# Kernel optimization log

Hardware: AMD Instinct MI355X
Metric: run time of the kernel (lower is better)

## Reference

```python
import jax, jax.numpy as jnp
import numpy as np

SEQ_LEN = 1024
DIM = 384
QK_DIM = 64
BATCH = 16


def setup_inputs() -> dict:
    key = jax.random.key(0)
    k_x, k_qw, k_qb, k_kw = jax.random.split(key, 4)
    bound = DIM ** (-0.5)
    x = jax.random.normal(k_x, (BATCH, SEQ_LEN, DIM), dtype=jnp.float32)
    # ColumnLinear params: weight [seq_len, out_features, in_features]
    q_weight = jax.random.uniform(k_qw, (SEQ_LEN, QK_DIM, DIM), minval=-bound, maxval=bound, dtype=jnp.float32)
    q_bias = jnp.zeros((SEQ_LEN, QK_DIM), dtype=jnp.float32)  # init zeros; keep as param
    k_weight = jax.random.uniform(k_kw, (SEQ_LEN, QK_DIM, DIM), minval=-bound, maxval=bound, dtype=jnp.float32)
    attn_bias = jnp.zeros((SEQ_LEN, SEQ_LEN), dtype=jnp.float32)
    return {"x": x, "q_weight": q_weight, "q_bias": q_bias, "k_weight": k_weight, "attn_bias": attn_bias}


def reference(x, q_weight, q_bias, k_weight, attn_bias):
    scale = DIM ** (-0.5)  # note: scale uses dim, not qk_dim
    # per-column (untied) linear projections
    q = scale * (jnp.einsum('bnc,ndc->bnd', x, q_weight) + q_bias)  # [B,S,qk]
    k = jnp.einsum('bnc,ndc->bnd', x, k_weight)                     # [B,S,qk]
    attn = jnp.einsum('bnd,bmd->bnm', q, k) + attn_bias             # [B,S,S]
    attn = jax.nn.softmax(attn, axis=-1)
    out = jnp.einsum('bnm,bmc->bnc', attn, x)                       # value = input
    return out, attn
```

## Files before the change

kernel.cpp:

```cpp
#include <hip/hip_runtime.h>

#define B_  16
#define S_  1024
#define D_  384
#define QK_ 64

typedef __attribute__((ext_vector_type(8))) short bf16x8;
typedef __attribute__((ext_vector_type(4))) short bf16x4;
typedef __attribute__((ext_vector_type(4))) float f32x4;

__device__ __forceinline__ short f2bf(float f) {
  union { float f; unsigned u; } v; v.f = f;
  unsigned r = v.u + 0x7FFFu + ((v.u >> 16) & 1u);
  return (short)(r >> 16);
}

__device__ __forceinline__ bf16x4 cvt4(const float4 v) {
  bf16x4 r;
  r[0] = f2bf(v.x); r[1] = f2bf(v.y); r[2] = f2bf(v.z); r[3] = f2bf(v.w);
  return r;
}

__global__ __launch_bounds__(256) void k_proj(
    const float* __restrict__ x, const float* __restrict__ qw,
    const float* __restrict__ qb, const float* __restrict__ kw,
    unsigned short* __restrict__ Qb, unsigned short* __restrict__ Kb) {
  __shared__ __attribute__((aligned(16))) short xs[16 * 392];
  __shared__ __attribute__((aligned(16))) short wsb[128 * 104];

  const int pos  = blockIdx.x;
  const int tid  = threadIdx.x;
  const int lane = tid & 63;
  const int w    = tid >> 6;
  const int col  = lane & 15;
  const int quad = lane >> 4;

#pragma unroll
  for (int r = 0; r < 6; ++r) {
    int li = tid + 256 * r;
    int brow = li / 96, c4 = li % 96;
    float4 v = *(const float4*)&x[(brow * S_ + pos) * D_ + 4 * c4];
    *(bf16x4*)&xs[brow * 392 + 4 * c4] = cvt4(v);
  }

  f32x4 acc0 = {0.f, 0.f, 0.f, 0.f};
  f32x4 acc1 = {0.f, 0.f, 0.f, 0.f};
  const int tt0 = 2 * w, tt1 = 2 * w + 1;

  for (int chunk = 0; chunk < 4; ++chunk) {
    const int c0 = chunk * 96;
    __syncthreads();
#pragma unroll
    for (int r = 0; r < 12; ++r) {
      int li = tid + 256 * r;
      int j = li / 24, c4 = li % 24;
      const float* src = (j < 64)
          ? &qw[(pos * 64 + j) * D_ + c0 + 4 * c4]
          : &kw[(pos * 64 + (j - 64)) * D_ + c0 + 4 * c4];
      *(bf16x4*)&wsb[j * 104 + 4 * c4] = cvt4(*(const float4*)src);
    }
    __syncthreads();
#pragma unroll
    for (int ks = 0; ks < 3; ++ks) {
      bf16x8 aF = *(const bf16x8*)&xs[col * 392 + c0 + ks * 32 + quad * 8];
      bf16x8 b0 = *(const bf16x8*)&wsb[(tt0 * 16 + col) * 104 + ks * 32 + quad * 8];
      bf16x8 b1 = *(const bf16x8*)&wsb[(tt1 * 16 + col) * 104 + ks * 32 + quad * 8];
      acc0 = __builtin_amdgcn_mfma_f32_16x16x32_bf16(aF, b0, acc0, 0, 0, 0);
      acc1 = __builtin_amdgcn_mfma_f32_16x16x32_bf16(aF, b1, acc1, 0, 0, 0);
    }
  }

  const float SCALE = 0.051031036307982884f;
#pragma unroll
  for (int a = 0; a < 2; ++a) {
    const f32x4 acc = a ? acc1 : acc0;
    const int tt = a ? tt1 : tt0;
    const int j = tt * 16 + col;
#pragma unroll
    for (int r = 0; r < 4; ++r) {
      const int brow = quad * 4 + r;
      float v = acc[r];
      if (j < 64) {
        v = SCALE * (v + qb[pos * 64 + j]);
        Qb[(brow * S_ + pos) * QK_ + j] = (unsigned short)f2bf(v);
      } else {
        Kb[(brow * S_ + pos) * QK_ + (j - 64)] = (unsigned short)f2bf(v);
      }
    }
  }
}

__global__ __launch_bounds__(256) void k_logits(
    const unsigned short* __restrict__ Qb, const unsigned short* __restrict__ Kb,
    const float* __restrict__ bias, float* __restrict__ attn) {
  __shared__ __attribute__((aligned(16))) short Qs[64 * 72];
  __shared__ __attribute__((aligned(16))) short Ks[64 * 72];
  const int gid = blockIdx.x;
  const int b = gid >> 8, it = (gid >> 4) & 15, jt = gid & 15;
  const int i0 = it * 64, j0 = jt * 64;
  const int tid = threadIdx.x, lane = tid & 63, w = tid >> 6;
  const int col = lane & 15, quad = lane >> 4;

#pragma unroll
  for (int r = 0; r < 2; ++r) {
    int li = tid + 256 * r;
    int row = li >> 3, q8 = li & 7;
    *(uint4*)&Qs[row * 72 + q8 * 8] =
        *(const uint4*)&Qb[(b * S_ + i0 + row) * QK_ + q8 * 8];
    *(uint4*)&Ks[row * 72 + q8 * 8] =
        *(const uint4*)&Kb[(b * S_ + j0 + row) * QK_ + q8 * 8];
  }
  __syncthreads();

  f32x4 acc[4] = {{0.f,0.f,0.f,0.f},{0.f,0.f,0.f,0.f},
                  {0.f,0.f,0.f,0.f},{0.f,0.f,0.f,0.f}};
#pragma unroll
  for (int ks = 0; ks < 2; ++ks) {
    bf16x8 aF = *(const bf16x8*)&Qs[(w * 16 + col) * 72 + ks * 32 + quad * 8];
#pragma unroll
    for (int s = 0; s < 4; ++s) {
      bf16x8 bF = *(const bf16x8*)&Ks[(s * 16 + col) * 72 + ks * 32 + quad * 8];
      acc[s] = __builtin_amdgcn_mfma_f32_16x16x32_bf16(aF, bF, acc[s], 0, 0, 0);
    }
  }
#pragma unroll
  for (int s = 0; s < 4; ++s) {
    const int j = j0 + s * 16 + col;
#pragma unroll
    for (int r = 0; r < 4; ++r) {
      const int i = i0 + w * 16 + quad * 4 + r;
      attn[(size_t)(b * S_ + i) * S_ + j] = acc[s][r] + bias[i * S_ + j];
    }
  }
}

__global__ __launch_bounds__(256) void k_softmax(float* __restrict__ attn) {
  const int tid = threadIdx.x, lane = tid & 63, w = tid >> 6;
  float* p = attn + (size_t)blockIdx.x * S_;
  float4 v = *(const float4*)&p[tid * 4];
  float m = fmaxf(fmaxf(v.x, v.y), fmaxf(v.z, v.w));
#pragma unroll
  for (int off = 32; off > 0; off >>= 1) m = fmaxf(m, __shfl_xor(m, off));
  __shared__ float redm[4], reds[4];
  if (lane == 0) redm[w] = m;
  __syncthreads();
  m = fmaxf(fmaxf(redm[0], redm[1]), fmaxf(redm[2], redm[3]));
  float4 e;
  e.x = __expf(v.x - m); e.y = __expf(v.y - m);
  e.z = __expf(v.z - m); e.w = __expf(v.w - m);
  float s = e.x + e.y + e.z + e.w;
#pragma unroll
  for (int off = 32; off > 0; off >>= 1) s += __shfl_xor(s, off);
  if (lane == 0) reds[w] = s;
  __syncthreads();
  s = reds[0] + reds[1] + reds[2] + reds[3];
  const float inv = 1.0f / s;
  e.x *= inv; e.y *= inv; e.z *= inv; e.w *= inv;
  *(float4*)&p[tid * 4] = e;
}

__global__ __launch_bounds__(256) void k_out(
    const float* __restrict__ attn, const float* __restrict__ x,
    float* __restrict__ out) {
  __shared__ __attribute__((aligned(16))) short Ps[64 * 40];
  __shared__ __attribute__((aligned(16))) short XsT[128 * 40];
  const int gid = blockIdx.x;
  const int b = gid / 48, r48 = gid % 48;
  const int it = r48 / 3, ct = r48 % 3;
  const int i0 = it * 64, c0 = ct * 128;
  const int tid = threadIdx.x, lane = tid & 63, w = tid >> 6;
  const int col = lane & 15, quad = lane >> 4;

  f32x4 acc[8] = {{0.f,0.f,0.f,0.f},{0.f,0.f,0.f,0.f},{0.f,0.f,0.f,0.f},
                  {0.f,0.f,0.f,0.f},{0.f,0.f,0.f,0.f},{0.f,0.f,0.f,0.f},
                  {0.f,0.f,0.f,0.f},{0.f,0.f,0.f,0.f}};

  for (int j0 = 0; j0 < S_; j0 += 32) {
    __syncthreads();
#pragma unroll
    for (int r = 0; r < 2; ++r) {
      int li = tid + 256 * r;
      int ii = li >> 3, f4 = li & 7;
      float4 v = *(const float4*)&attn[(size_t)(b * S_ + i0 + ii) * S_ + j0 + f4 * 4];
      *(bf16x4*)&Ps[ii * 40 + f4 * 4] = cvt4(v);
    }
#pragma unroll
    for (int r = 0; r < 4; ++r) {
      int li = tid + 256 * r;
      int jj = li >> 5, f4 = li & 31;
      float4 v = *(const float4*)&x[(b * S_ + j0 + jj) * D_ + c0 + f4 * 4];
      XsT[(f4 * 4 + 0) * 40 + jj] = f2bf(v.x);
      XsT[(f4 * 4 + 1) * 40 + jj] = f2bf(v.y);
      XsT[(f4 * 4 + 2) * 40 + jj] = f2bf(v.z);
      XsT[(f4 * 4 + 3) * 40 + jj] = f2bf(v.w);
    }
    __syncthreads();
    bf16x8 aF = *(const bf16x8*)&Ps[(w * 16 + col) * 40 + quad * 8];
#pragma unroll
    for (int s = 0; s < 8; ++s) {
      bf16x8 bF = *(const bf16x8*)&XsT[(s * 16 + col) * 40 + quad * 8];
      acc[s] = __builtin_amdgcn_mfma_f32_16x16x32_bf16(aF, bF, acc[s], 0, 0, 0);
    }
  }
#pragma unroll
  for (int s = 0; s < 8; ++s) {
    const int c = c0 + s * 16 + col;
#pragma unroll
    for (int r = 0; r < 4; ++r) {
      const int i = i0 + w * 16 + quad * 4 + r;
      out[(size_t)(b * S_ + i) * D_ + c] = acc[s][r];
    }
  }
}

extern "C" void kernel_launch(void* const* d_in, const int* in_sizes, int n_in,
                              void* d_out, int out_size, void* d_ws, size_t ws_size,
                              hipStream_t stream) {
  const float* x  = (const float*)d_in[0];
  const float* qw = (const float*)d_in[1];
  const float* qb = (const float*)d_in[2];
  const float* kw = (const float*)d_in[3];
  const float* ab = (const float*)d_in[4];

  float* out  = (float*)d_out;
  float* attn = out + (size_t)B_ * S_ * D_;

  unsigned short* Qb = (unsigned short*)d_ws;
  unsigned short* Kb = Qb + (size_t)B_ * S_ * QK_;

  k_proj   <<<S_,          256, 0, stream>>>(x, qw, qb, kw, Qb, Kb);
  k_logits <<<B_ * 16 * 16, 256, 0, stream>>>(Qb, Kb, ab, attn);
  k_softmax<<<B_ * S_,     256, 0, stream>>>(attn);
  k_out    <<<B_ * 16 * 3, 256, 0, stream>>>(attn, x, out);
}
```

Measured before the change: 416.8 us.

## Split projection blocks, pre-transpose x to bf16, and pipeline k_out loads

The projection kernel now launches two blocks per position, one for Q and one for K, and reads weights directly from global memory into MFMA operands without staging them in LDS. A new k_xt kernel writes a bf16 transposed copy of x once, so k_out no longer converts and transposes x in every tile. k_out now uses 64-wide K steps with register prefetch of the next tile, overlapping global loads with MFMA work. k_logits and k_out also remap block indices, presumably to spread batches across XCDs and improve cache locality. The cost is an extra kernel launch, extra workspace traffic for the transposed x, and higher register use from the prefetch buffers.

```diff
diff --git a/kernel.cpp b/kernel.cpp
--- a/kernel.cpp
+++ b/kernel.cpp
@@ -26,9 +26,9 @@
     const float* __restrict__ qb, const float* __restrict__ kw,
     unsigned short* __restrict__ Qb, unsigned short* __restrict__ Kb) {
   __shared__ __attribute__((aligned(16))) short xs[16 * 392];
-  __shared__ __attribute__((aligned(16))) short wsb[128 * 104];
-
-  const int pos  = blockIdx.x;
+
+  const int pos  = blockIdx.x >> 1;
+  const int half = blockIdx.x & 1;
   const int tid  = threadIdx.x;
   const int lane = tid & 63;
   const int w    = tid >> 6;
@@ -42,51 +42,56 @@
     float4 v = *(const float4*)&x[(brow * S_ + pos) * D_ + 4 * c4];
     *(bf16x4*)&xs[brow * 392 + 4 * c4] = cvt4(v);
   }
-
-  f32x4 acc0 = {0.f, 0.f, 0.f, 0.f};
-  f32x4 acc1 = {0.f, 0.f, 0.f, 0.f};
-  const int tt0 = 2 * w, tt1 = 2 * w + 1;
-
-  for (int chunk = 0; chunk < 4; ++chunk) {
-    const int c0 = chunk * 96;
-    __syncthreads();
-#pragma unroll
-    for (int r = 0; r < 12; ++r) {
-      int li = tid + 256 * r;
-      int j = li / 24, c4 = li % 24;
-      const float* src = (j < 64)
-          ? &qw[(pos * 64 + j) * D_ + c0 + 4 * c4]
-          : &kw[(pos * 64 + (j - 64)) * D_ + c0 + 4 * c4];
-      *(bf16x4*)&wsb[j * 104 + 4 * c4] = cvt4(*(const float4*)src);
-    }
-    __syncthreads();
-#pragma unroll
-    for (int ks = 0; ks < 3; ++ks) {
-      bf16x8 aF = *(const bf16x8*)&xs[col * 392 + c0 + ks * 32 + quad * 8];
-      bf16x8 b0 = *(const bf16x8*)&wsb[(tt0 * 16 + col) * 104 + ks * 32 + quad * 8];
-      bf16x8 b1 = *(const bf16x8*)&wsb[(tt1 * 16 + col) * 104 + ks * 32 + quad * 8];
-      acc0 = __builtin_amdgcn_mfma_f32_16x16x32_bf16(aF, b0, acc0, 0, 0, 0);
-      acc1 = __builtin_amdgcn_mfma_f32_16x16x32_bf16(aF, b1, acc1, 0, 0, 0);
-    }
+  __syncthreads();
+
+  const float* wsrc = half ? kw : qw;
+  const int j = w * 16 + col;
+  const float* wrow = &wsrc[((size_t)pos * QK_ + j) * D_];
+
+  f32x4 acc = {0.f, 0.f, 0.f, 0.f};
+#pragma unroll
+  for (int ks = 0; ks < 12; ++ks) {
+    bf16x8 aF = *(const bf16x8*)&xs[col * 392 + ks * 32 + quad * 8];
+    float4 w0 = *(const float4*)&wrow[ks * 32 + quad * 8];
+    float4 w1 = *(const float4*)&wrow[ks * 32 + quad * 8 + 4];
+    bf16x4 lo = cvt4(w0), hi = cvt4(w1);
+    bf16x8 bF;
+    bF[0] = lo[0]; bF[1] = lo[1]; bF[2] = lo[2]; bF[3] = lo[3];
+    bF[4] = hi[0]; bF[5] = hi[1]; bF[6] = hi[2]; bF[7] = hi[3];
+    acc = __builtin_amdgcn_mfma_f32_16x16x32_bf16(aF, bF, acc, 0, 0, 0);
   }
 
   const float SCALE = 0.051031036307982884f;
 #pragma unroll
-  for (int a = 0; a < 2; ++a) {
-    const f32x4 acc = a ? acc1 : acc0;
-    const int tt = a ? tt1 : tt0;
-    const int j = tt * 16 + col;
-#pragma unroll
-    for (int r = 0; r < 4; ++r) {
-      const int brow = quad * 4 + r;
-      float v = acc[r];
-      if (j < 64) {
-        v = SCALE * (v + qb[pos * 64 + j]);
-        Qb[(brow * S_ + pos) * QK_ + j] = (unsigned short)f2bf(v);
-      } else {
-        Kb[(brow * S_ + pos) * QK_ + (j - 64)] = (unsigned short)f2bf(v);
-      }
-    }
+  for (int r = 0; r < 4; ++r) {
+    const int brow = quad * 4 + r;
+    float v = acc[r];
+    if (half == 0) {
+      v = SCALE * (v + qb[pos * QK_ + j]);
+      Qb[(brow * S_ + pos) * QK_ + j] = (unsigned short)f2bf(v);
+    } else {
+      Kb[(brow * S_ + pos) * QK_ + j] = (unsigned short)f2bf(v);
+    }
+  }
+}
+
+__global__ __launch_bounds__(256) void k_xt(
+    const float* __restrict__ x, unsigned short* __restrict__ Xt) {
+  __shared__ float T[32][33];
+  const int gid = blockIdx.x;
+  const int b  = gid / (32 * 12);
+  const int r  = gid % (32 * 12);
+  const int jt = r / 12, ct = r % 12;
+  const int j0 = jt * 32, c0 = ct * 32;
+  const int tx = threadIdx.x & 31, ty = threadIdx.x >> 5;
+#pragma unroll
+  for (int k = 0; k < 4; ++k)
+    T[ty + 8 * k][tx] = x[(size_t)(b * S_ + j0 + ty + 8 * k) * D_ + c0 + tx];
+  __syncthreads();
+#pragma unroll
+  for (int k = 0; k < 4; ++k) {
+    int c = ty + 8 * k;
+    Xt[((size_t)b * D_ + c0 + c) * S_ + j0 + tx] = (unsigned short)f2bf(T[tx][c]);
   }
 }
 
@@ -95,7 +100,8 @@
     const float* __restrict__ bias, float* __restrict__ attn) {
   __shared__ __attribute__((aligned(16))) short Qs[64 * 72];
   __shared__ __attribute__((aligned(16))) short Ks[64 * 72];
-  const int gid = blockIdx.x;
+  const int gid0 = blockIdx.x;
+  const int gid  = (gid0 & 7) * 512 + (gid0 >> 3);
   const int b = gid >> 8, it = (gid >> 4) & 15, jt = gid & 15;
   const int i0 = it * 64, j0 = jt * 64;
   const int tid = threadIdx.x, lane = tid & 63, w = tid >> 6;
@@ -160,48 +166,74 @@
 }
 
 __global__ __launch_bounds__(256) void k_out(
-    const float* __restrict__ attn, const float* __restrict__ x,
+    const float* __restrict__ attn, const unsigned short* __restrict__ Xt,
     float* __restrict__ out) {
-  __shared__ __attribute__((aligned(16))) short Ps[64 * 40];
-  __shared__ __attribute__((aligned(16))) short XsT[128 * 40];
-  const int gid = blockIdx.x;
+  __shared__ __attribute__((aligned(16))) short Ps[64 * 72];
+  __shared__ __attribute__((aligned(16))) short Xs[128 * 72];
+  const int gid0 = blockIdx.x;
+  const int gid  = (gid0 & 7) * 96 + (gid0 >> 3);
   const int b = gid / 48, r48 = gid % 48;
   const int it = r48 / 3, ct = r48 % 3;
   const int i0 = it * 64, c0 = ct * 128;
   const int tid = threadIdx.x, lane = tid & 63, w = tid >> 6;
   const int col = lane & 15, quad = lane >> 4;
 
+  const float* pA = &attn[(size_t)(b * S_ + i0) * S_];
+  const unsigned short* xA = &Xt[((size_t)b * D_ + c0) * S_];
+
   f32x4 acc[8] = {{0.f,0.f,0.f,0.f},{0.f,0.f,0.f,0.f},{0.f,0.f,0.f,0.f},
                   {0.f,0.f,0.f,0.f},{0.f,0.f,0.f,0.f},{0.f,0.f,0.f,0.f},
                   {0.f,0.f,0.f,0.f},{0.f,0.f,0.f,0.f}};
 
-  for (int j0 = 0; j0 < S_; j0 += 32) {
+  float4 pv[4];
+  uint4  xv[4];
+
+#pragma unroll
+  for (int r = 0; r < 4; ++r) {
+    int li = tid + 256 * r;
+    { int ii = li >> 4, f4 = li & 15;
+      pv[r] = *(const float4*)&pA[(size_t)ii * S_ + f4 * 4]; }
+    { int cc = li >> 3, p8 = li & 7;
+      xv[r] = *(const uint4*)&xA[(size_t)cc * S_ + p8 * 8]; }
+  }
+
+  for (int t = 0; t < 16; ++t) {
     __syncthreads();
 #pragma unroll
-    for (int r = 0; r < 2; ++r) {
+    for (int r = 0; r < 4; ++r) {
       int li = tid + 256 * r;
-      int ii = li >> 3, f4 = li & 7;
-      float4 v = *(const float4*)&attn[(size_t)(b * S_ + i0 + ii) * S_ + j0 + f4 * 4];
-      *(bf16x4*)&Ps[ii * 40 + f4 * 4] = cvt4(v);
+      int ii = li >> 4, f4 = li & 15;
+      *(bf16x4*)&Ps[ii * 72 + f4 * 4] = cvt4(pv[r]);
     }
 #pragma unroll
     for (int r = 0; r < 4; ++r) {
       int li = tid + 256 * r;
-      int jj = li >> 5, f4 = li & 31;
-      float4 v = *(const float4*)&x[(b * S_ + j0 + jj) * D_ + c0 + f4 * 4];
-      XsT[(f4 * 4 + 0) * 40 + jj] = f2bf(v.x);
-      XsT[(f4 * 4 + 1) * 40 + jj] = f2bf(v.y);
-      XsT[(f4 * 4 + 2) * 40 + jj] = f2bf(v.z);
-      XsT[(f4 * 4 + 3) * 40 + jj] = f2bf(v.w);
+      int cc = li >> 3, p8 = li & 7;
+      *(uint4*)&Xs[cc * 72 + p8 * 8] = xv[r];
     }
     __syncthreads();
-    bf16x8 aF = *(const bf16x8*)&Ps[(w * 16 + col) * 40 + quad * 8];
-#pragma unroll
-    for (int s = 0; s < 8; ++s) {
-      bf16x8 bF = *(const bf16x8*)&XsT[(s * 16 + col) * 40 + quad * 8];
-      acc[s] = __builtin_amdgcn_mfma_f32_16x16x32_bf16(aF, bF, acc[s], 0, 0, 0);
-    }
-  }
+    if (t < 15) {
+      const int j1 = (t + 1) * 64;
+#pragma unroll
+      for (int r = 0; r < 4; ++r) {
+        int li = tid + 256 * r;
+        { int ii = li >> 4, f4 = li & 15;
+          pv[r] = *(const float4*)&pA[(size_t)ii * S_ + j1 + f4 * 4]; }
+        { int cc = li >> 3, p8 = li & 7;
+          xv[r] = *(const uint4*)&xA[(size_t)cc * S_ + j1 + p8 * 8]; }
+      }
+    }
+#pragma unroll
+    for (int ks = 0; ks < 2; ++ks) {
+      bf16x8 aF = *(const bf16x8*)&Ps[(w * 16 + col) * 72 + ks * 32 + quad * 8];
+#pragma unroll
+      for (int s = 0; s < 8; ++s) {
+        bf16x8 bF = *(const bf16x8*)&Xs[(s * 16 + col) * 72 + ks * 32 + quad * 8];
+        acc[s] = __builtin_amdgcn_mfma_f32_16x16x32_bf16(aF, bF, acc[s], 0, 0, 0);
+      }
+    }
+  }
+
 #pragma unroll
   for (int s = 0; s < 8; ++s) {
     const int c = c0 + s * 16 + col;
@@ -227,9 +259,11 @@
 
   unsigned short* Qb = (unsigned short*)d_ws;
   unsigned short* Kb = Qb + (size_t)B_ * S_ * QK_;
-
-  k_proj   <<<S_,          256, 0, stream>>>(x, qw, qb, kw, Qb, Kb);
-  k_logits <<<B_ * 16 * 16, 256, 0, stream>>>(Qb, Kb, ab, attn);
-  k_softmax<<<B_ * S_,     256, 0, stream>>>(attn);
-  k_out    <<<B_ * 16 * 3, 256, 0, stream>>>(attn, x, out);
-}
+  unsigned short* Xt = Kb + (size_t)B_ * S_ * QK_;
+
+  k_proj   <<<2 * S_,        256, 0, stream>>>(x, qw, qb, kw, Qb, Kb);
+  k_xt     <<<B_ * 32 * 12,  256, 0, stream>>>(x, Xt);
+  k_logits <<<B_ * 16 * 16,  256, 0, stream>>>(Qb, Kb, ab, attn);
+  k_softmax<<<B_ * S_,       256, 0, stream>>>(attn);
+  k_out    <<<B_ * 16 * 3,   256, 0, stream>>>(attn, Xt, out);
+}
```

Measured after the change: 381.4 us. 1.09x faster.
